# Optimization experiments

Measured on AMD Instinct MI355X. Metric: run time of the kernel, lower is better.

Reference implementation:

```python
import jax, jax.numpy as jnp
import numpy as np

N_NODES = 50000
N_EDGES = 600000
IN_F, HID_F, OUT_F = 128, 128, 64


def setup_inputs() -> dict:
    key = jax.random.key(0)
    ks = jax.random.split(key, 7)
    features = jax.random.normal(ks[0], (N_NODES, IN_F), jnp.float32)
    W1 = jax.random.normal(ks[1], (IN_F, HID_F), jnp.float32) / np.sqrt(IN_F)
    b1 = jnp.zeros((HID_F,), jnp.float32)
    W2 = jax.random.normal(ks[2], (HID_F, OUT_F), jnp.float32) / np.sqrt(HID_F)
    b2 = jnp.zeros((OUT_F,), jnp.float32)
    edge_src = jax.random.randint(ks[3], (N_EDGES,), 0, N_NODES, jnp.int32)
    edge_dst = jax.random.randint(ks[4], (N_EDGES,), 0, N_NODES, jnp.int32)
    return {"features": features, "W1": W1, "b1": b1, "W2": W2, "b2": b2,
            "edge_src": edge_src, "edge_dst": edge_dst}


def _graph_conv(h, W, b, edge_src, edge_dst, norm_src, norm_dst, n_nodes):
    # DGL GraphConv, norm='both': D_in^{-1/2} A D_out^{-1/2} (h W) + b
    # Apply W first (linear commutes with the linear aggregation) to minimize
    # the size of the gathered edge tensor when out <= in.
    h = (h * norm_src[:, None]) @ W                       # [N, d_out]
    agg = jax.ops.segment_sum(h[edge_src], edge_dst, num_segments=n_nodes)
    return agg * norm_dst[:, None] + b


def reference(features, W1, b1, W2, b2, edge_src, edge_dst):
    n_nodes = features.shape[0]
    ones = jnp.ones(edge_src.shape[0], features.dtype)
    out_deg = jax.ops.segment_sum(ones, edge_src, num_segments=n_nodes)
    in_deg = jax.ops.segment_sum(ones, edge_dst, num_segments=n_nodes)
    norm_src = jnp.clip(out_deg, 1.0) ** -0.5             # source-side D_out^{-1/2}
    norm_dst = jnp.clip(in_deg, 1.0) ** -0.5              # dest-side   D_in^{-1/2}
    h = _graph_conv(features, W1, b1, edge_src, edge_dst, norm_src, norm_dst, n_nodes)
    h = jax.nn.relu(h)
    h = _graph_conv(h, W2, b2, edge_src, edge_dst, norm_src, norm_dst, n_nodes)
    return h
```

## Files before the change

kernel.cpp:

```cpp
#include <hip/hip_runtime.h>


typedef unsigned short u16;
typedef unsigned int u32;
typedef short s16x8 __attribute__((ext_vector_type(8)));
typedef float f32x4 __attribute__((ext_vector_type(4)));

__device__ __forceinline__ float bf2f(u16 u) {
    return __uint_as_float((u32)u << 16);
}
__device__ __forceinline__ u16 f2bf(float f) {
    u32 u = __float_as_uint(f);
    u += 0x7fff + ((u >> 16) & 1);
    return (u16)(u >> 16);
}
__device__ __forceinline__ s16x8 frag4(const u32 p0, const u32 p1,
                                       const u32 p2, const u32 p3) {
    union { u32 u[4]; s16x8 v; } x;
    x.u[0] = p0; x.u[1] = p1; x.u[2] = p2; x.u[3] = p3;
    return x.v;
}


__global__ __launch_bounds__(256) void hist_part(const int* __restrict__ src,
                                                 const int* __restrict__ dst,
                                                 u32* __restrict__ part) {
    __shared__ u32 cnt[6250];
    const int s = blockIdx.x;
    const int r = blockIdx.y;
    const int z = blockIdx.z;
    const int lo = r * 12500;
    for (int t = threadIdx.x; t < 6250; t += 256) cnt[t] = 0;
    __syncthreads();
    const int* ids = z ? dst : src;
    const int base = s * 37500;
    for (int e0 = base; e0 < base + 37500; e0 += 1024) {
        int idx[4];
#pragma unroll
        for (int k = 0; k < 4; ++k) {
            int e = e0 + k * 256 + threadIdx.x;
            idx[k] = (e < base + 37500) ? ids[e] : -1;
        }
#pragma unroll
        for (int k = 0; k < 4; ++k) {
            unsigned local = (unsigned)(idx[k] - lo);
            if (local < 12500u)
                atomicAdd(&cnt[local >> 1], 1u << ((local & 1) * 16));
        }
    }
    __syncthreads();
    u32* out = part + (size_t)(z * 16 + s) * 25000 + r * 6250;
    for (int t = threadIdx.x; t < 6250; t += 256) out[t] = cnt[t];
}

__global__ __launch_bounds__(256) void reduce_sniff(const u32* __restrict__ part,
                                                    int* __restrict__ degs,
                                                    int* __restrict__ degd,
                                                    const u16* __restrict__ X16,
                                                    int* __restrict__ flag) {
    if (blockIdx.x == 0) {
        __shared__ int sh[256];
        u16 v = X16[threadIdx.x * 2];
        int e = (v >> 7) & 0xFF;
        sh[threadIdx.x] = (e >= 0x30 && e <= 0x47) ? 1 : 0;
        __syncthreads();
        for (int off = 128; off > 0; off >>= 1) {
            if (threadIdx.x < off) sh[threadIdx.x] += sh[threadIdx.x + off];
            __syncthreads();
        }
        if (threadIdx.x == 0) *flag = (sh[0] >= 128) ? 1 : 0;
    }
    int i = blockIdx.x * 256 + threadIdx.x;
    if (i >= 50000) return;
    const int w = i >> 1, h = (i & 1) * 16;
    u32 a = 0, b = 0;
#pragma unroll
    for (int s = 0; s < 16; ++s) {
        a += (part[(size_t)s * 25000 + w] >> h) & 0xffffu;
        b += (part[(size_t)(16 + s) * 25000 + w] >> h) & 0xffffu;
    }
    degs[i] = (int)a;
    degd[i] = (int)b;
}

__global__ __launch_bounds__(256) void blocksum_norm_kernel(const int* __restrict__ degs,
                                                            const int* __restrict__ degd,
                                                            float* ns, float* nd,
                                                            int* __restrict__ bsum, int n) {
    __shared__ int sh[256];
    int i = blockIdx.x * 256 + threadIdx.x;
    int v = (i < n) ? degd[i] : 0;
    if (i < n) {
        int a = degs[i] > 1 ? degs[i] : 1;
        int b = v > 1 ? v : 1;
        ns[i] = rsqrtf((float)a);
        nd[i] = rsqrtf((float)b);
    }
    sh[threadIdx.x] = v;
    __syncthreads();
    for (int off = 128; off > 0; off >>= 1) {
        if (threadIdx.x < off) sh[threadIdx.x] += sh[threadIdx.x + off];
        __syncthreads();
    }
    if (threadIdx.x == 0) bsum[blockIdx.x] = sh[0];
}

__global__ __launch_bounds__(256) void scan_blocks_kernel(const int* __restrict__ bsum,
                                                          int* __restrict__ boffs,
                                                          int nb, int* __restrict__ total) {
    __shared__ int sh[256];
    int v = (threadIdx.x < nb) ? bsum[threadIdx.x] : 0;
    sh[threadIdx.x] = v;
    __syncthreads();
    for (int off = 1; off < 256; off <<= 1) {
        int x = (threadIdx.x >= off) ? sh[threadIdx.x - off] : 0;
        __syncthreads();
        sh[threadIdx.x] += x;
        __syncthreads();
    }
    if (threadIdx.x < nb) boffs[threadIdx.x] = sh[threadIdx.x] - v;
    if (threadIdx.x == 255) *total = sh[255];
}

__global__ __launch_bounds__(256) void rowptr_kernel(const int* __restrict__ deg,
                                                     const int* __restrict__ boffs,
                                                     int* __restrict__ rp,
                                                     int* __restrict__ cur, int n) {
    __shared__ int sh[256];
    int i = blockIdx.x * 256 + threadIdx.x;
    int v = (i < n) ? deg[i] : 0;
    sh[threadIdx.x] = v;
    __syncthreads();
    for (int off = 1; off < 256; off <<= 1) {
        int x = (threadIdx.x >= off) ? sh[threadIdx.x - off] : 0;
        __syncthreads();
        sh[threadIdx.x] += x;
        __syncthreads();
    }
    if (i < n) {
        int e = boffs[blockIdx.x] + sh[threadIdx.x] - v;
        rp[i] = e;
        cur[i] = e;
    }
}

__global__ __launch_bounds__(256) void fill_kernel(const int* __restrict__ src,
                                                   const int* __restrict__ dst,
                                                   int* __restrict__ cur,
                                                   int* __restrict__ col, int n) {
    int i = blockIdx.x * 256 + threadIdx.x;
    if (i < n) {
        int pos = atomicAdd(&cur[dst[i]], 1);
        col[pos] = src[i];
    }
}

template <int FO, bool X_ALWAYS_BF16>
__global__ __launch_bounds__(256) void gemm_mfma(const void* __restrict__ Xv,
                                                 const void* __restrict__ Wv,
                                                 const int* __restrict__ flagp,
                                                 const float* __restrict__ ns,
                                                 u16* __restrict__ Ylo,
                                                 u16* __restrict__ Yhi,
                                                 int split, int nrows) {
    constexpr int BS = FO + 5;
    __shared__ u32 Xs[64 * 65];
    __shared__ u32 Bs[64 * BS];
    const int flag = *flagp;
    const int tid = threadIdx.x;
    const int nb = blockIdx.x * 64;

    const bool xbf = X_ALWAYS_BF16 ? true : (flag != 0);
    if (xbf) {
        const u32* Xg = (const u32*)Xv;
        for (int t = tid; t < 64 * 64; t += 256) {
            int row = t >> 6, cp = t & 63;
            int r = nb + row;
            Xs[row * 65 + cp] = (r < nrows) ? Xg[(size_t)r * 64 + cp] : 0u;
        }
    } else {
        const float* Xg = (const float*)Xv;
        for (int t = tid; t < 64 * 64; t += 256) {
            int row = t >> 6, cp = t & 63;
            int r = nb + row;
            u32 lo = 0, hi = 0;
            if (r < nrows) {
                lo = f2bf(Xg[(size_t)r * 128 + 2 * cp]);
                hi = f2bf(Xg[(size_t)r * 128 + 2 * cp + 1]);
            }
            Xs[row * 65 + cp] = lo | (hi << 16);
        }
    }
    if (flag) {
        const u32* Wg = (const u32*)Wv;
        for (int t = tid; t < 64 * FO; t += 256) {
            int kp = t / FO, col = t % FO;
            u32 lo = Wg[(size_t)(2 * kp) * (FO / 2) + (col >> 1)];
            u32 hi = Wg[(size_t)(2 * kp + 1) * (FO / 2) + (col >> 1)];
            int sh = (col & 1) * 16;
            Bs[kp * BS + col] = ((lo >> sh) & 0xffffu) | (((hi >> sh) & 0xffffu) << 16);
        }
    } else {
        const float* Wg = (const float*)Wv;
        for (int t = tid; t < 64 * FO; t += 256) {
            int kp = t / FO, col = t % FO;
            u32 lo = f2bf(Wg[(size_t)(2 * kp) * FO + col]);
            u32 hi = f2bf(Wg[(size_t)(2 * kp + 1) * FO + col]);
            Bs[kp * BS + col] = lo | (hi << 16);
        }
    }
    __syncthreads();

    const int lane = tid & 63;
    const int wv = tid >> 6;
    const int rt = wv * 16;
    const int lr = lane & 15;
    const int g = lane >> 4;

    u32 a[4][4];
#pragma unroll
    for (int t = 0; t < 4; ++t)
#pragma unroll
        for (int p = 0; p < 4; ++p)
            a[t][p] = Xs[(rt + lr) * 65 + t * 16 + g * 4 + p];

    const int rq = nb + rt + g * 4;
    float nsv[4];
#pragma unroll
    for (int q = 0; q < 4; ++q) nsv[q] = ns[rq + q];

#pragma unroll
    for (int ct = 0; ct < FO / 16; ++ct) {
        f32x4 acc = {0.f, 0.f, 0.f, 0.f};
#pragma unroll
        for (int t = 0; t < 4; ++t) {
            u32 b0 = Bs[(t * 16 + g * 4 + 0) * BS + ct * 16 + lr];
            u32 b1 = Bs[(t * 16 + g * 4 + 1) * BS + ct * 16 + lr];
            u32 b2 = Bs[(t * 16 + g * 4 + 2) * BS + ct * 16 + lr];
            u32 b3 = Bs[(t * 16 + g * 4 + 3) * BS + ct * 16 + lr];
            acc = __builtin_amdgcn_mfma_f32_16x16x32_bf16(
                frag4(a[t][0], a[t][1], a[t][2], a[t][3]),
                frag4(b0, b1, b2, b3), acc, 0, 0, 0);
        }
        const int cc = ct * 16 + lr;
#pragma unroll
        for (int q = 0; q < 4; ++q) {
            int r = rq + q;
            if (r < nrows) {
                u16* Y = (r < split) ? (Ylo + (size_t)r * FO)
                                     : (Yhi + (size_t)(r - split) * FO);
                Y[cc] = f2bf(acc[q] * nsv[q]);
            }
        }
    }
}

__global__ __launch_bounds__(256) void gather128(const u16* __restrict__ Hlo,
                                                 const u16* __restrict__ Hhi, int split,
                                                 const int* __restrict__ rp,
                                                 const int* __restrict__ col,
                                                 const float* __restrict__ nd,
                                                 const void* __restrict__ bias,
                                                 const int* __restrict__ flagp,
                                                 u16* __restrict__ out, int nnodes) {
    int wv = threadIdx.x >> 6, lane = threadIdx.x & 63;
    int n = blockIdx.x * 4 + wv;
    if (n >= nnodes) return;
    int p0 = rp[n], p1 = rp[n + 1];
    float a0 = 0.f, a1 = 0.f;
    int e = p0;
    for (; e + 8 <= p1; e += 8) {
        u32 u[8];
#pragma unroll
        for (int t = 0; t < 8; ++t) {
            int s = col[e + t];
            const u32* r = (const u32*)((s < split) ? (Hlo + (size_t)s * 128)
                                                    : (Hhi + (size_t)(s - split) * 128));
            u[t] = r[lane];
        }
#pragma unroll
        for (int t = 0; t < 8; ++t) {
            a0 += bf2f((u16)(u[t] & 0xffff));
            a1 += bf2f((u16)(u[t] >> 16));
        }
    }
    for (; e + 4 <= p1; e += 4) {
        u32 u[4];
#pragma unroll
        for (int t = 0; t < 4; ++t) {
            int s = col[e + t];
            const u32* r = (const u32*)((s < split) ? (Hlo + (size_t)s * 128)
                                                    : (Hhi + (size_t)(s - split) * 128));
            u[t] = r[lane];
        }
#pragma unroll
        for (int t = 0; t < 4; ++t) {
            a0 += bf2f((u16)(u[t] & 0xffff));
            a1 += bf2f((u16)(u[t] >> 16));
        }
    }
    for (; e < p1; ++e) {
        int s = col[e];
        const u16* H = (s < split) ? (Hlo + (size_t)s * 128)
                                   : (Hhi + (size_t)(s - split) * 128);
        u32 u = ((const u32*)H)[lane];
        a0 += bf2f((u16)(u & 0xffff));
        a1 += bf2f((u16)(u >> 16));
    }
    int flag = *flagp;
    float bb0 = flag ? bf2f(((const u16*)bias)[lane * 2]) : ((const float*)bias)[lane * 2];
    float bb1 = flag ? bf2f(((const u16*)bias)[lane * 2 + 1]) : ((const float*)bias)[lane * 2 + 1];
    float v = nd[n];
    float o0 = fmaxf(a0 * v + bb0, 0.f);
    float o1 = fmaxf(a1 * v + bb1, 0.f);
    ((u32*)(out + (size_t)n * 128))[lane] = (u32)f2bf(o0) | ((u32)f2bf(o1) << 16);
}

__global__ __launch_bounds__(256) void gather64(const u16* __restrict__ H,
                                                const int* __restrict__ rp,
                                                const int* __restrict__ col,
                                                const float* __restrict__ nd,
                                                const void* __restrict__ bias,
                                                const int* __restrict__ flagp,
                                                void* __restrict__ outv, int nnodes) {
    int wv = threadIdx.x >> 6, lane = threadIdx.x & 63;
    int n = blockIdx.x * 4 + wv;
    if (n >= nnodes) return;
    int p0 = rp[n], p1 = rp[n + 1];
    float a = 0.f;
    int e = p0;
    for (; e + 8 <= p1; e += 8) {
        float f[8];
#pragma unroll
        for (int t = 0; t < 8; ++t)
            f[t] = bf2f(H[(size_t)col[e + t] * 64 + lane]);
#pragma unroll
        for (int t = 0; t < 8; ++t) a += f[t];
    }
    for (; e + 4 <= p1; e += 4) {
        float f[4];
#pragma unroll
        for (int t = 0; t < 4; ++t)
            f[t] = bf2f(H[(size_t)col[e + t] * 64 + lane]);
#pragma unroll
        for (int t = 0; t < 4; ++t) a += f[t];
    }
    for (; e < p1; ++e)
        a += bf2f(H[(size_t)col[e] * 64 + lane]);
    int flag = *flagp;
    float bb = flag ? bf2f(((const u16*)bias)[lane]) : ((const float*)bias)[lane];
    float o = a * nd[n] + bb;
    if (flag)
        ((u16*)outv)[(size_t)n * 64 + lane] = f2bf(o);
    else
        ((float*)outv)[(size_t)n * 64 + lane] = o;
}

extern "C" void kernel_launch(void* const* d_in, const int* in_sizes, int n_in,
                              void* d_out, int out_size, void* d_ws, size_t ws_size,
                              hipStream_t stream) {
    constexpr int N = 50000;
    constexpr int E = 600000;
    constexpr int NB = (N + 255) / 256;
    constexpr int SPLIT = 25000;

    const void* X  = d_in[0];
    const void* W1 = d_in[1];
    const void* b1 = d_in[2];
    const void* W2 = d_in[3];
    const void* b2 = d_in[4];
    const int* esrc = (const int*)d_in[5];
    const int* edst = (const int*)d_in[6];

    char* p = (char*)d_ws;
    auto take = [&](size_t bytes) -> char* {
        char* r = p;
        p += (bytes + 255) & ~(size_t)255;
        return r;
    };
    int* flagp  = (int*)take(256);
    int* deg_s  = (int*)take((size_t)N * 4);
    int* deg_d  = (int*)take((size_t)N * 4);
    float* ns   = (float*)take((size_t)N * 4);
    float* nd   = (float*)take((size_t)N * 4);
    int* bsum   = (int*)take((size_t)NB * 4);
    int* boffs  = (int*)take((size_t)NB * 4);
    int* rp     = (int*)take((size_t)(N + 1) * 4);
    int* cur    = (int*)take((size_t)N * 4);
    int* col    = (int*)take((size_t)E * 4);
    u16* h0hi   = (u16*)take((size_t)(N - SPLIT) * 128 * 2);
    u16* a2     = (u16*)take((size_t)N * 128 * 2);
    size_t NEED = (size_t)(p - (char*)d_ws);

    if (ws_size < NEED) {
        hipMemsetAsync(d_out, 0, (size_t)out_size * 2, stream);
        return;
    }

    u16* h0lo = (u16*)d_out;

    u32* part = (u32*)a2;

    hist_part<<<dim3(16, 4, 2), 256, 0, stream>>>(esrc, edst, part);
    reduce_sniff<<<NB, 256, 0, stream>>>(part, deg_s, deg_d, (const u16*)X, flagp);
    blocksum_norm_kernel<<<NB, 256, 0, stream>>>(deg_s, deg_d, ns, nd, bsum, N);
    scan_blocks_kernel<<<1, 256, 0, stream>>>(bsum, boffs, NB, rp + N);
    rowptr_kernel<<<NB, 256, 0, stream>>>(deg_d, boffs, rp, cur, N);
    fill_kernel<<<(E + 255) / 256, 256, 0, stream>>>(esrc, edst, cur, col, E);

    gemm_mfma<128, false><<<(N + 63) / 64, 256, 0, stream>>>(
        X, W1, flagp, ns, h0lo, h0hi, SPLIT, N);
    gather128<<<(N + 3) / 4, 256, 0, stream>>>(h0lo, h0hi, SPLIT, rp, col, nd,
                                               b1, flagp, a2, N);

    u16* h1b = h0hi;
    gemm_mfma<64, true><<<(N + 63) / 64, 256, 0, stream>>>(
        a2, W2, flagp, ns, h1b, h1b, N, N);
    gather64<<<(N + 3) / 4, 256, 0, stream>>>(h1b, rp, col, nd, b2, flagp,
                                              d_out, N);

    (void)in_sizes; (void)n_in; (void)out_size;
}
```

Measured before the change: 239.2 us.

## Fuse degree/norm/scan kernels and vectorize MFMA LDS operand loads

```diff
diff --git a/kernel.cpp b/kernel.cpp
--- a/kernel.cpp
+++ b/kernel.cpp
@@ -5,6 +5,7 @@
 typedef unsigned int u32;
 typedef short s16x8 __attribute__((ext_vector_type(8)));
 typedef float f32x4 __attribute__((ext_vector_type(4)));
+typedef u32 u32x4 __attribute__((ext_vector_type(4)));
 
 __device__ __forceinline__ float bf2f(u16 u) {
     return __uint_as_float((u32)u << 16);
@@ -13,12 +14,6 @@
     u32 u = __float_as_uint(f);
     u += 0x7fff + ((u >> 16) & 1);
     return (u16)(u >> 16);
-}
-__device__ __forceinline__ s16x8 frag4(const u32 p0, const u32 p1,
-                                       const u32 p2, const u32 p3) {
-    union { u32 u[4]; s16x8 v; } x;
-    x.u[0] = p0; x.u[1] = p1; x.u[2] = p2; x.u[3] = p3;
-    return x.v;
 }
 
 
@@ -53,13 +48,15 @@
     for (int t = threadIdx.x; t < 6250; t += 256) out[t] = cnt[t];
 }
 
-__global__ __launch_bounds__(256) void reduce_sniff(const u32* __restrict__ part,
-                                                    int* __restrict__ degs,
-                                                    int* __restrict__ degd,
-                                                    const u16* __restrict__ X16,
-                                                    int* __restrict__ flag) {
+__global__ __launch_bounds__(256) void reduce_norm_sniff(const u32* __restrict__ part,
+                                                         int* __restrict__ degd,
+                                                         float* __restrict__ ns,
+                                                         float* __restrict__ nd,
+                                                         int* __restrict__ bsum,
+                                                         const u16* __restrict__ X16,
+                                                         int* __restrict__ flag) {
+    __shared__ int sh[256];
     if (blockIdx.x == 0) {
-        __shared__ int sh[256];
         u16 v = X16[threadIdx.x * 2];
         int e = (v >> 7) & 0xFF;
         sh[threadIdx.x] = (e >= 0x30 && e <= 0x47) ? 1 : 0;
@@ -69,34 +66,22 @@
             __syncthreads();
         }
         if (threadIdx.x == 0) *flag = (sh[0] >= 128) ? 1 : 0;
+        __syncthreads();
     }
     int i = blockIdx.x * 256 + threadIdx.x;
-    if (i >= 50000) return;
-    const int w = i >> 1, h = (i & 1) * 16;
     u32 a = 0, b = 0;
-#pragma unroll
-    for (int s = 0; s < 16; ++s) {
-        a += (part[(size_t)s * 25000 + w] >> h) & 0xffffu;
-        b += (part[(size_t)(16 + s) * 25000 + w] >> h) & 0xffffu;
-    }
-    degs[i] = (int)a;
-    degd[i] = (int)b;
-}
-
-__global__ __launch_bounds__(256) void blocksum_norm_kernel(const int* __restrict__ degs,
-                                                            const int* __restrict__ degd,
-                                                            float* ns, float* nd,
-                                                            int* __restrict__ bsum, int n) {
-    __shared__ int sh[256];
-    int i = blockIdx.x * 256 + threadIdx.x;
-    int v = (i < n) ? degd[i] : 0;
-    if (i < n) {
-        int a = degs[i] > 1 ? degs[i] : 1;
-        int b = v > 1 ? v : 1;
-        ns[i] = rsqrtf((float)a);
-        nd[i] = rsqrtf((float)b);
-    }
-    sh[threadIdx.x] = v;
+    if (i < 50000) {
+        const int w = i >> 1, h = (i & 1) * 16;
+#pragma unroll
+        for (int s = 0; s < 16; ++s) {
+            a += (part[(size_t)s * 25000 + w] >> h) & 0xffffu;
+            b += (part[(size_t)(16 + s) * 25000 + w] >> h) & 0xffffu;
+        }
+        degd[i] = (int)b;
+        ns[i] = rsqrtf((float)(a > 1 ? a : 1));
+        nd[i] = rsqrtf((float)(b > 1 ? b : 1));
+    }
+    sh[threadIdx.x] = (i < 50000) ? (int)b : 0;
     __syncthreads();
     for (int off = 128; off > 0; off >>= 1) {
         if (threadIdx.x < off) sh[threadIdx.x] += sh[threadIdx.x + off];
@@ -105,42 +90,35 @@
     if (threadIdx.x == 0) bsum[blockIdx.x] = sh[0];
 }
 
-__global__ __launch_bounds__(256) void scan_blocks_kernel(const int* __restrict__ bsum,
-                                                          int* __restrict__ boffs,
-                                                          int nb, int* __restrict__ total) {
+__global__ __launch_bounds__(256) void rowptr_scan(const int* __restrict__ degd,
+                                                   const int* __restrict__ bsum,
+                                                   int* __restrict__ rp,
+                                                   int* __restrict__ cur,
+                                                   int n, int nb) {
+    __shared__ int sb[256];
     __shared__ int sh[256];
-    int v = (threadIdx.x < nb) ? bsum[threadIdx.x] : 0;
-    sh[threadIdx.x] = v;
-    __syncthreads();
+    const int t = threadIdx.x;
+    sb[t] = (t < nb && t < (int)blockIdx.x) ? bsum[t] : 0;
+    int i = blockIdx.x * 256 + t;
+    int v = (i < n) ? degd[i] : 0;
+    sh[t] = v;
+    __syncthreads();
+    for (int off = 128; off > 0; off >>= 1) {
+        if (t < off) sb[t] += sb[t + off];
+        __syncthreads();
+    }
+    const int boff = sb[0];
     for (int off = 1; off < 256; off <<= 1) {
-        int x = (threadIdx.x >= off) ? sh[threadIdx.x - off] : 0;
-        __syncthreads();
-        sh[threadIdx.x] += x;
-        __syncthreads();
-    }
-    if (threadIdx.x < nb) boffs[threadIdx.x] = sh[threadIdx.x] - v;
-    if (threadIdx.x == 255) *total = sh[255];
-}
-
-__global__ __launch_bounds__(256) void rowptr_kernel(const int* __restrict__ deg,
-                                                     const int* __restrict__ boffs,
-                                                     int* __restrict__ rp,
-                                                     int* __restrict__ cur, int n) {
-    __shared__ int sh[256];
-    int i = blockIdx.x * 256 + threadIdx.x;
-    int v = (i < n) ? deg[i] : 0;
-    sh[threadIdx.x] = v;
-    __syncthreads();
-    for (int off = 1; off < 256; off <<= 1) {
-        int x = (threadIdx.x >= off) ? sh[threadIdx.x - off] : 0;
-        __syncthreads();
-        sh[threadIdx.x] += x;
+        int x = (t >= off) ? sh[t - off] : 0;
+        __syncthreads();
+        sh[t] += x;
         __syncthreads();
     }
     if (i < n) {
-        int e = boffs[blockIdx.x] + sh[threadIdx.x] - v;
+        int e = boff + sh[t] - v;
         rp[i] = e;
         cur[i] = e;
+        if (i == n - 1) rp[n] = e + v;
     }
 }
 
@@ -163,9 +141,8 @@
                                                  u16* __restrict__ Ylo,
                                                  u16* __restrict__ Yhi,
                                                  int split, int nrows) {
-    constexpr int BS = FO + 5;
-    __shared__ u32 Xs[64 * 65];
-    __shared__ u32 Bs[64 * BS];
+    __shared__ __align__(16) u32 Xs[64 * 68];
+    __shared__ __align__(16) u32 Bs[FO * 68];
     const int flag = *flagp;
     const int tid = threadIdx.x;
     const int nb = blockIdx.x * 64;
@@ -176,7 +153,7 @@
         for (int t = tid; t < 64 * 64; t += 256) {
             int row = t >> 6, cp = t & 63;
             int r = nb + row;
-            Xs[row * 65 + cp] = (r < nrows) ? Xg[(size_t)r * 64 + cp] : 0u;
+            Xs[row * 68 + cp] = (r < nrows) ? Xg[(size_t)r * 64 + cp] : 0u;
         }
     } else {
         const float* Xg = (const float*)Xv;
@@ -188,25 +165,25 @@
                 lo = f2bf(Xg[(size_t)r * 128 + 2 * cp]);
                 hi = f2bf(Xg[(size_t)r * 128 + 2 * cp + 1]);
             }
-            Xs[row * 65 + cp] = lo | (hi << 16);
+            Xs[row * 68 + cp] = lo | (hi << 16);
         }
     }
     if (flag) {
         const u32* Wg = (const u32*)Wv;
-        for (int t = tid; t < 64 * FO; t += 256) {
-            int kp = t / FO, col = t % FO;
+        for (int t = tid; t < FO * 64; t += 256) {
+            int col = t >> 6, kp = t & 63;
             u32 lo = Wg[(size_t)(2 * kp) * (FO / 2) + (col >> 1)];
             u32 hi = Wg[(size_t)(2 * kp + 1) * (FO / 2) + (col >> 1)];
             int sh = (col & 1) * 16;
-            Bs[kp * BS + col] = ((lo >> sh) & 0xffffu) | (((hi >> sh) & 0xffffu) << 16);
+            Bs[col * 68 + kp] = ((lo >> sh) & 0xffffu) | (((hi >> sh) & 0xffffu) << 16);
         }
     } else {
         const float* Wg = (const float*)Wv;
-        for (int t = tid; t < 64 * FO; t += 256) {
-            int kp = t / FO, col = t % FO;
+        for (int t = tid; t < FO * 64; t += 256) {
+            int col = t >> 6, kp = t & 63;
             u32 lo = f2bf(Wg[(size_t)(2 * kp) * FO + col]);
             u32 hi = f2bf(Wg[(size_t)(2 * kp + 1) * FO + col]);
-            Bs[kp * BS + col] = lo | (hi << 16);
+            Bs[col * 68 + kp] = lo | (hi << 16);
         }
     }
     __syncthreads();
@@ -217,12 +194,12 @@
     const int lr = lane & 15;
     const int g = lane >> 4;
 
-    u32 a[4][4];
+    union U4 { u32x4 u; s16x8 s; };
+
+    U4 a[4];
 #pragma unroll
     for (int t = 0; t < 4; ++t)
-#pragma unroll
-        for (int p = 0; p < 4; ++p)
-            a[t][p] = Xs[(rt + lr) * 65 + t * 16 + g * 4 + p];
+        a[t].u = *(const u32x4*)&Xs[(rt + lr) * 68 + t * 16 + g * 4];
 
     const int rq = nb + rt + g * 4;
     float nsv[4];
@@ -234,13 +211,10 @@
         f32x4 acc = {0.f, 0.f, 0.f, 0.f};
 #pragma unroll
         for (int t = 0; t < 4; ++t) {
-            u32 b0 = Bs[(t * 16 + g * 4 + 0) * BS + ct * 16 + lr];
-            u32 b1 = Bs[(t * 16 + g * 4 + 1) * BS + ct * 16 + lr];
-            u32 b2 = Bs[(t * 16 + g * 4 + 2) * BS + ct * 16 + lr];
-            u32 b3 = Bs[(t * 16 + g * 4 + 3) * BS + ct * 16 + lr];
-            acc = __builtin_amdgcn_mfma_f32_16x16x32_bf16(
-                frag4(a[t][0], a[t][1], a[t][2], a[t][3]),
-                frag4(b0, b1, b2, b3), acc, 0, 0, 0);
+            U4 b;
+            b.u = *(const u32x4*)&Bs[(ct * 16 + lr) * 68 + t * 16 + g * 4];
+            acc = __builtin_amdgcn_mfma_f32_16x16x32_bf16(a[t].s, b.s, acc,
+                                                          0, 0, 0);
         }
         const int cc = ct * 16 + lr;
 #pragma unroll
@@ -379,12 +353,10 @@
         return r;
     };
     int* flagp  = (int*)take(256);
-    int* deg_s  = (int*)take((size_t)N * 4);
     int* deg_d  = (int*)take((size_t)N * 4);
     float* ns   = (float*)take((size_t)N * 4);
     float* nd   = (float*)take((size_t)N * 4);
     int* bsum   = (int*)take((size_t)NB * 4);
-    int* boffs  = (int*)take((size_t)NB * 4);
     int* rp     = (int*)take((size_t)(N + 1) * 4);
     int* cur    = (int*)take((size_t)N * 4);
     int* col    = (int*)take((size_t)E * 4);
@@ -402,10 +374,9 @@
     u32* part = (u32*)a2;
 
     hist_part<<<dim3(16, 4, 2), 256, 0, stream>>>(esrc, edst, part);
-    reduce_sniff<<<NB, 256, 0, stream>>>(part, deg_s, deg_d, (const u16*)X, flagp);
-    blocksum_norm_kernel<<<NB, 256, 0, stream>>>(deg_s, deg_d, ns, nd, bsum, N);
-    scan_blocks_kernel<<<1, 256, 0, stream>>>(bsum, boffs, NB, rp + N);
-    rowptr_kernel<<<NB, 256, 0, stream>>>(deg_d, boffs, rp, cur, N);
+    reduce_norm_sniff<<<NB, 256, 0, stream>>>(part, deg_d, ns, nd, bsum,
+                                              (const u16*)X, flagp);
+    rowptr_scan<<<NB, 256, 0, stream>>>(deg_d, bsum, rp, cur, N, NB);
     fill_kernel<<<(E + 255) / 256, 256, 0, stream>>>(esrc, edst, cur, col, E);
 
     gemm_mfma<128, false><<<(N + 63) / 64, 256, 0, stream>>>(
```

New measurement: 265.6 us. 1.11x slower.
